# Performance work log

Hardware: AMD Instinct MI355X
Metric: run time of the kernel (lower is better)

The kernel has to match this reference:

```python
import jax, jax.numpy as jnp
import numpy as np

H = 768
T = 512
NC = 8          # chunks -> encoding has NC*T rows
NL = 8921       # ICD label set size
NN = 4          # number of notes
NEG = -1e9      # finite stand-in for float('-inf') mask (avoids NaN from all--inf softmax columns)


def setup_inputs() -> dict:
    key = jax.random.key(0)
    k1, k2, k3, k4 = jax.random.split(key, 4)
    encoding = jax.random.normal(k1, (NC * T, H), dtype=jnp.float32)
    label_queries = 0.1 * jax.random.normal(k2, (H, NL), dtype=jnp.float32)
    label_weights = 0.1 * jax.random.normal(k3, (H, NL), dtype=jnp.float32)
    note_end_chunk_ids = jnp.sort(jax.random.randint(k4, (NN,), 0, NC, dtype=jnp.int64))
    return {
        "encoding": encoding,
        "label_queries": label_queries,
        "label_weights": label_weights,
        "note_end_chunk_ids": note_end_chunk_ids,
        "seq_len": T,
    }


def reference(encoding, label_queries, label_weights, note_end_chunk_ids, seq_len):
    NcT, h = encoding.shape          # (Nc*T, H)
    Nn = note_end_chunk_ids.shape[0]
    Nl = label_queries.shape[1]
    # mask[i, p] = NEG for p < (id_i + 1) * T, else 0  (vectorized version of the torch loop)
    pos = jnp.arange(NcT)
    mask = jnp.where(pos[None, :] < (note_end_chunk_ids + 1)[:, None] * seq_len,
                     jnp.float32(NEG), jnp.float32(0.0))          # (Nn, Nc*T)
    scores = encoding @ label_queries                              # (Nc*T, Nl)
    scores = scores[None, :, :] + mask[:, :, None]                 # (Nn, Nc*T, Nl)
    # softmax over the note dimension (dim=0), as in the original
    weights = jax.nn.softmax(scores, axis=0)
    # torch .view(Nn, Nl, Nc*T) is a raw row-major reshape, NOT a transpose
    values = jnp.reshape(weights, (Nn, Nl, NcT)) @ encoding        # (Nn, Nl, H)
    # label_weights.view(1, Nl, H): raw reshape of the (H, Nl) buffer
    lw = jnp.reshape(label_weights, (1, Nl, h))
    score = jnp.sum(values * lw, axis=1)                           # (Nn, H)
    return jax.nn.sigmoid(score)
```

## Files before the change

### kernel.cpp

```cpp
#include <hip/hip_runtime.h>
#include <hip/hip_bf16.h>
#include <math.h>

#define HD      768
#define TLEN    512
#define NCH     8
#define NLBL    8921
#define NNOTE   4
#define NCT     4096
#define ROWK    1115
#define F4      192

#define ENC_BLOCKS      64
#define ENC_SEGS        8
#define ENC_ROWS        64
#define LW_SEGS_PER_K   24
#define LW_ROWS         48
#define LW_BLOCKS       (NCH * LW_SEGS_PER_K)
#define NPART           (ENC_BLOCKS + LW_BLOCKS)

__global__ __launch_bounds__(192) void talc_reduce_kernel(
    const float* __restrict__ enc,
    const float* __restrict__ lw,
    float* __restrict__ ws) {
  const int t = threadIdx.x;
  const int b = blockIdx.x;
  float4* P = (float4*)ws;

  const float4* base;
  int rn;
  if (b < ENC_BLOCKS) {
    const int c = b >> 3;
    const int seg = b & 7;
    base = (const float4*)enc + (size_t)(c * TLEN + seg * ENC_ROWS) * F4 + t;
    rn = ENC_ROWS;
  } else {
    const int bb = b - ENC_BLOCKS;
    const int k = bb / LW_SEGS_PER_K;
    const int seg = bb % LW_SEGS_PER_K;
    base = (const float4*)lw + (size_t)(k * ROWK + seg * LW_ROWS) * F4 + t;
    rn = (seg == LW_SEGS_PER_K - 1) ? (ROWK - (LW_SEGS_PER_K - 1) * LW_ROWS)
                                    : LW_ROWS;
  }

  float4 acc = make_float4(0.f, 0.f, 0.f, 0.f);
#pragma unroll 8
  for (int r = 0; r < rn; ++r) {
    float4 v = base[(size_t)r * F4];
    acc.x += v.x; acc.y += v.y; acc.z += v.z; acc.w += v.w;
  }
  P[(size_t)b * F4 + t] = acc;
}

__global__ __launch_bounds__(128) void talc_finish_kernel(
    const float* __restrict__ lw,
    const int* __restrict__ ids,
    const float* __restrict__ ws,
    float* __restrict__ out) {
  const int h = blockIdx.x * 128 + threadIdx.x;
  if (h >= HD) return;
  const float* P = ws;

  float B[NCH];
#pragma unroll
  for (int c = 0; c < NCH; ++c) {
    float s = 0.f;
#pragma unroll
    for (int g = 0; g < ENC_SEGS; ++g) s += P[(size_t)(c * ENC_SEGS + g) * HD + h];
    B[c] = s;
  }
  float Esuf[NCH + 1];
  Esuf[NCH] = 0.f;
#pragma unroll
  for (int c = NCH - 1; c >= 0; --c) Esuf[c] = Esuf[c + 1] + B[c];
  float Epre[NCH + 1];
  Epre[0] = 0.f;
#pragma unroll
  for (int c = 1; c <= NCH; ++c) Epre[c] = Epre[c - 1] + B[c - 1];
  const float E = Esuf[0];

  float Tk[NCH];
#pragma unroll
  for (int k = 0; k < NCH; ++k) {
    float s = 0.f;
#pragma unroll
    for (int g = 0; g < LW_SEGS_PER_K; ++g)
      s += P[(size_t)(ENC_BLOCKS + k * LW_SEGS_PER_K + g) * HD + h];
    Tk[k] = s;
  }

  float R[NCH + 1];
#pragma unroll
  for (int m = 0; m <= NCH; ++m) R[m] = lw[(size_t)(m * ROWK) * HD + h];

  float G[NCH];
#pragma unroll
  for (int k = 0; k < NCH; ++k) {
    G[k] = R[k] * Esuf[k] + (Tk[k] - R[k]) * E + R[k + 1] * Epre[k + 1];
  }

  int id[NNOTE];
#pragma unroll
  for (int n = 0; n < NNOTE; ++n) id[n] = ids[n];

  float score[NNOTE] = {0.f, 0.f, 0.f, 0.f};
#pragma unroll
  for (int c = 0; c < NCH; ++c) {
    int cnt = 0;
#pragma unroll
    for (int n = 0; n < NNOTE; ++n) cnt += (id[n] + 1 <= c) ? 1 : 0;
    const float inv = (cnt > 0) ? (1.f / (float)cnt) : 0.f;
#pragma unroll
    for (int n = 0; n < NNOTE; ++n) {
      const float m = (cnt == 0) ? 0.25f : (((id[n] + 1) <= c) ? inv : 0.f);
      score[n] += m * G[c];
    }
  }
#pragma unroll
  for (int n = 0; n < NNOTE; ++n) {
    out[(size_t)n * HD + h] = 1.f / (1.f + expf(-score[n]));
  }
}

extern "C" void kernel_launch(void* const* d_in, const int* in_sizes, int n_in,
                              void* d_out, int out_size, void* d_ws, size_t ws_size,
                              hipStream_t stream) {
  const float* enc = (const float*)d_in[0];
  const float* lw  = (const float*)d_in[2];
  const int*   ids = (const int*)d_in[3];
  float* ws  = (float*)d_ws;
  float* out = (float*)d_out;

  talc_reduce_kernel<<<NPART, 192, 0, stream>>>(enc, lw, ws);
  talc_finish_kernel<<<6, 128, 0, stream>>>(lw, ids, ws, out);
}
```

Measured before the change: 104.3 us.

## Fuse reduce and finish kernels via atomic counters and last-block tree reduction

Merges the partial-sum reduction and the finishing kernel into one launch. The last blocks wait on global atomic counters: 16 blocks do a second-level reduction of partials and 4 blocks compute the final scores and sigmoid. Block count and segment sizes are rebalanced to 256 blocks, one per CU. The aim is to remove the second kernel launch and the serial finish pass. In exchange it adds a memset launch and spin-wait barriers that assume all blocks are co-resident on the device.

```diff
diff --git a/kernel.cpp b/kernel.cpp
--- a/kernel.cpp
+++ b/kernel.cpp
@@ -1,136 +1,163 @@
 #include <hip/hip_runtime.h>
-#include <hip/hip_bf16.h>
 #include <math.h>
 
 #define HD      768
 #define TLEN    512
 #define NCH     8
-#define NLBL    8921
 #define NNOTE   4
-#define NCT     4096
 #define ROWK    1115
 #define F4      192
 
-#define ENC_BLOCKS      64
-#define ENC_SEGS        8
-#define ENC_ROWS        64
-#define LW_SEGS_PER_K   24
-#define LW_ROWS         48
-#define LW_BLOCKS       (NCH * LW_SEGS_PER_K)
-#define NPART           (ENC_BLOCKS + LW_BLOCKS)
+#define ENC_BLOCKS  80
+#define LW_BLOCKS   176
+#define NPART       256
 
-__global__ __launch_bounds__(192) void talc_reduce_kernel(
+#define WS2_OFF     (NPART * HD)
+#define CNT_OFF     (WS2_OFF + 16 * HD)
+#define FIN0        240
+#define FIN1        252
+
+__global__ __launch_bounds__(192) void talc_fused_kernel(
     const float* __restrict__ enc,
     const float* __restrict__ lw,
-    float* __restrict__ ws) {
+    const int* __restrict__ ids,
+    float* __restrict__ ws,
+    float* __restrict__ out) {
   const int t = threadIdx.x;
   const int b = blockIdx.x;
-  float4* P = (float4*)ws;
+  float4* P  = (float4*)ws;
+  float4* W2 = (float4*)(ws + WS2_OFF);
+  unsigned* cnt = (unsigned*)(ws + CNT_OFF);
 
-  const float4* base;
-  int rn;
-  if (b < ENC_BLOCKS) {
-    const int c = b >> 3;
-    const int seg = b & 7;
-    base = (const float4*)enc + (size_t)(c * TLEN + seg * ENC_ROWS) * F4 + t;
-    rn = ENC_ROWS;
-  } else {
-    const int bb = b - ENC_BLOCKS;
-    const int k = bb / LW_SEGS_PER_K;
-    const int seg = bb % LW_SEGS_PER_K;
-    base = (const float4*)lw + (size_t)(k * ROWK + seg * LW_ROWS) * F4 + t;
-    rn = (seg == LW_SEGS_PER_K - 1) ? (ROWK - (LW_SEGS_PER_K - 1) * LW_ROWS)
-                                    : LW_ROWS;
+  {
+    const float4* base;
+    int rn;
+    if (b < ENC_BLOCKS) {
+      const int c = b / 10, seg = b - c * 10;
+      const int start = (seg < 8) ? 51 * seg : 408 + 52 * (seg - 8);
+      rn = (seg < 8) ? 51 : 52;
+      base = (const float4*)enc + (size_t)(c * TLEN + start) * F4 + t;
+    } else {
+      const int l = b - ENC_BLOCKS;
+      const int k = l / 22, seg = l - k * 22;
+      const int start = (seg < 15) ? 51 * seg : 765 + 50 * (seg - 15);
+      rn = (seg < 15) ? 51 : 50;
+      base = (const float4*)lw + (size_t)(k * ROWK + start) * F4 + t;
+    }
+    float4 acc = make_float4(0.f, 0.f, 0.f, 0.f);
+#pragma unroll 8
+    for (int r = 0; r < rn; ++r) {
+      float4 v = base[(size_t)r * F4];
+      acc.x += v.x; acc.y += v.y; acc.z += v.z; acc.w += v.w;
+    }
+    P[(size_t)b * F4 + t] = acc;
   }
+  __syncthreads();
+  if (t == 0) {
+    __threadfence();
+    atomicAdd(&cnt[0], 1u);
+  }
+  if (b < FIN0) return;
 
-  float4 acc = make_float4(0.f, 0.f, 0.f, 0.f);
-#pragma unroll 8
-  for (int r = 0; r < rn; ++r) {
-    float4 v = base[(size_t)r * F4];
-    acc.x += v.x; acc.y += v.y; acc.z += v.z; acc.w += v.w;
+  if (t == 0) {
+    while (__hip_atomic_load(&cnt[0], __ATOMIC_RELAXED, __HIP_MEMORY_SCOPE_AGENT) < NPART)
+      __builtin_amdgcn_s_sleep(8);
   }
-  P[(size_t)b * F4 + t] = acc;
-}
+  __syncthreads();
+  __builtin_amdgcn_fence(__ATOMIC_ACQUIRE, "agent");
+  {
+    const int f = b - FIN0;
+    float4 s = make_float4(0.f, 0.f, 0.f, 0.f);
+    if (f < 8) {
+#pragma unroll
+      for (int g = 0; g < 10; ++g) {
+        float4 v = P[(size_t)(f * 10 + g) * F4 + t];
+        s.x += v.x; s.y += v.y; s.z += v.z; s.w += v.w;
+      }
+    } else {
+#pragma unroll
+      for (int g = 0; g < 22; ++g) {
+        float4 v = P[(size_t)(ENC_BLOCKS + (f - 8) * 22 + g) * F4 + t];
+        s.x += v.x; s.y += v.y; s.z += v.z; s.w += v.w;
+      }
+    }
+    W2[(size_t)f * F4 + t] = s;
+  }
+  __syncthreads();
+  if (t == 0) {
+    __threadfence();
+    atomicAdd(&cnt[1], 1u);
+  }
+  if (b < FIN1) return;
 
-__global__ __launch_bounds__(128) void talc_finish_kernel(
-    const float* __restrict__ lw,
-    const int* __restrict__ ids,
-    const float* __restrict__ ws,
-    float* __restrict__ out) {
-  const int h = blockIdx.x * 128 + threadIdx.x;
-  if (h >= HD) return;
-  const float* P = ws;
+  if (t == 0) {
+    while (__hip_atomic_load(&cnt[1], __ATOMIC_RELAXED, __HIP_MEMORY_SCOPE_AGENT) < 16u)
+      __builtin_amdgcn_s_sleep(8);
+  }
+  __syncthreads();
+  __builtin_amdgcn_fence(__ATOMIC_ACQUIRE, "agent");
+  {
+    const int h = (b - FIN1) * 192 + t;
+    const float* ws2 = ws + WS2_OFF;
 
-  float B[NCH];
+    float B[NCH], Tk[NCH];
 #pragma unroll
-  for (int c = 0; c < NCH; ++c) {
-    float s = 0.f;
+    for (int c = 0; c < NCH; ++c) B[c] = ws2[(size_t)c * HD + h];
 #pragma unroll
-    for (int g = 0; g < ENC_SEGS; ++g) s += P[(size_t)(c * ENC_SEGS + g) * HD + h];
-    B[c] = s;
-  }
-  float Esuf[NCH + 1];
-  Esuf[NCH] = 0.f;
+    for (int k = 0; k < NCH; ++k) Tk[k] = ws2[(size_t)(8 + k) * HD + h];
+
+    float Esuf[NCH + 1];
+    Esuf[NCH] = 0.f;
 #pragma unroll
-  for (int c = NCH - 1; c >= 0; --c) Esuf[c] = Esuf[c + 1] + B[c];
-  float Epre[NCH + 1];
-  Epre[0] = 0.f;
+    for (int c = NCH - 1; c >= 0; --c) Esuf[c] = Esuf[c + 1] + B[c];
+    float Epre[NCH + 1];
+    Epre[0] = 0.f;
 #pragma unroll
-  for (int c = 1; c <= NCH; ++c) Epre[c] = Epre[c - 1] + B[c - 1];
-  const float E = Esuf[0];
+    for (int c = 1; c <= NCH; ++c) Epre[c] = Epre[c - 1] + B[c - 1];
+    const float E = Esuf[0];
 
-  float Tk[NCH];
+    float R[NCH + 1];
 #pragma unroll
-  for (int k = 0; k < NCH; ++k) {
-    float s = 0.f;
+    for (int m = 0; m <= NCH; ++m) R[m] = lw[(size_t)(m * ROWK) * HD + h];
+
+    float G[NCH];
 #pragma unroll
-    for (int g = 0; g < LW_SEGS_PER_K; ++g)
-      s += P[(size_t)(ENC_BLOCKS + k * LW_SEGS_PER_K + g) * HD + h];
-    Tk[k] = s;
-  }
+    for (int k = 0; k < NCH; ++k)
+      G[k] = R[k] * Esuf[k] + (Tk[k] - R[k]) * E + R[k + 1] * Epre[k + 1];
 
-  float R[NCH + 1];
+    int id[NNOTE];
 #pragma unroll
-  for (int m = 0; m <= NCH; ++m) R[m] = lw[(size_t)(m * ROWK) * HD + h];
+    for (int n = 0; n < NNOTE; ++n) id[n] = ids[n];
 
-  float G[NCH];
+    float score[NNOTE] = {0.f, 0.f, 0.f, 0.f};
 #pragma unroll
-  for (int k = 0; k < NCH; ++k) {
-    G[k] = R[k] * Esuf[k] + (Tk[k] - R[k]) * E + R[k + 1] * Epre[k + 1];
-  }
-
-  int id[NNOTE];
+    for (int c = 0; c < NCH; ++c) {
+      int cm = 0;
 #pragma unroll
-  for (int n = 0; n < NNOTE; ++n) id[n] = ids[n];
-
-  float score[NNOTE] = {0.f, 0.f, 0.f, 0.f};
+      for (int n = 0; n < NNOTE; ++n) cm += (id[n] + 1 <= c) ? 1 : 0;
+      const float inv = (cm > 0) ? (1.f / (float)cm) : 0.f;
 #pragma unroll
-  for (int c = 0; c < NCH; ++c) {
-    int cnt = 0;
+      for (int n = 0; n < NNOTE; ++n) {
+        const float m = (cm == 0) ? 0.25f : (((id[n] + 1) <= c) ? inv : 0.f);
+        score[n] += m * G[c];
+      }
+    }
 #pragma unroll
-    for (int n = 0; n < NNOTE; ++n) cnt += (id[n] + 1 <= c) ? 1 : 0;
-    const float inv = (cnt > 0) ? (1.f / (float)cnt) : 0.f;
-#pragma unroll
-    for (int n = 0; n < NNOTE; ++n) {
-      const float m = (cnt == 0) ? 0.25f : (((id[n] + 1) <= c) ? inv : 0.f);
-      score[n] += m * G[c];
-    }
-  }
-#pragma unroll
-  for (int n = 0; n < NNOTE; ++n) {
-    out[(size_t)n * HD + h] = 1.f / (1.f + expf(-score[n]));
+    for (int n = 0; n < NNOTE; ++n)
+      out[(size_t)n * HD + h] = 1.f / (1.f + expf(-score[n]));
   }
 }
 
 extern "C" void kernel_launch(void* const* d_in, const int* in_sizes, int n_in,
                               void* d_out, int out_size, void* d_ws, size_t ws_size,
                               hipStream_t stream) {
+  (void)in_sizes; (void)n_in; (void)out_size; (void)ws_size;
   const float* enc = (const float*)d_in[0];
   const float* lw  = (const float*)d_in[2];
   const int*   ids = (const int*)d_in[3];
   float* ws  = (float*)d_ws;
   float* out = (float*)d_out;
 
-  talc_reduce_kernel<<<NPART, 192, 0, stream>>>(enc, lw, ws);
-  talc_finish_kernel<<<6, 128, 0, stream>>>(lw, ids, ws, out);
+  hipMemsetAsync((char*)d_ws + (size_t)CNT_OFF * 4, 0, 8, stream);
+  talc_fused_kernel<<<NPART, 192, 0, stream>>>(enc, lw, ids, ws, out);
 }
```

Measured after the change: 115.9 us. 1.11x slower.
